# Optimization experiments

Hardware: AMD Instinct MI355X
Metric: run time of the kernel (lower is better)

Reference implementation:

```python
import jax, jax.numpy as jnp
from jax import lax
import numpy as np

B, N, NPOINT, NSAMPLE, C = 4, 8192, 2048, 32, 128
RADIUS = 0.2
H1, H2, OUT = 64, 128, 128  # mlp: (3+C)->H1->H2, sas: H2->OUT


def fps(xyz, npoint):
    # furthest point sampling: xyz (B,N,3) -> idx (B,npoint) int32
    b, n, _ = xyz.shape
    init_idx = jnp.zeros((b,), jnp.int32)

    def step(carry, _):
        dist, last = carry
        p = jnp.take_along_axis(xyz, last[:, None, None], axis=1)  # (B,1,3)
        d = jnp.sum((xyz - p) ** 2, axis=-1)                       # (B,N)
        dist = jnp.minimum(dist, d)
        nxt = jnp.argmax(dist, axis=-1).astype(jnp.int32)
        return (dist, nxt), nxt

    (_, _), rest = lax.scan(step, (jnp.full((b, n), 1e10, jnp.float32), init_idx),
                            None, length=npoint - 1)
    return jnp.concatenate([init_idx[None, :], rest], axis=0).T    # (B,npoint)


def ball_query(xyz, new_xyz, radius, nsample):
    # xyz (B,N,3), new_xyz (B,S,3) -> idx (B,S,nsample) int32
    n = xyz.shape[1]
    d2 = jnp.sum((new_xyz[:, :, None, :] - xyz[:, None, :, :]) ** 2, axis=-1)  # (B,S,N)
    ar = jnp.arange(n, dtype=jnp.int32)
    keys = jnp.where(d2 <= radius * radius, ar, n)  # valid -> own index, invalid -> N
    neg_vals, _ = lax.top_k(-keys, nsample)          # smallest nsample keys
    idx = -neg_vals
    first = idx[..., :1]
    return jnp.where(idx >= n, first, idx)           # pad invalid with first valid


def gather_points(pts, idx):
    # pts (B,N,D), idx (B,S,ns) -> (B,S,ns,D)
    b, s, ns = idx.shape
    flat = jnp.take_along_axis(pts, idx.reshape(b, s * ns, 1), axis=1)
    return flat.reshape(b, s, ns, -1)


def setup_inputs() -> dict:
    key = jax.random.key(0)
    ks = jax.random.split(key, 8)
    xyz = jax.random.uniform(ks[0], (B, N, 3), dtype=jnp.float32)
    features = jax.random.normal(ks[1], (B, C, N), dtype=jnp.float32)
    cin = C + 3
    W1 = jax.random.normal(ks[2], (H1, cin), dtype=jnp.float32) / np.sqrt(cin)
    b1 = jnp.zeros((H1,), jnp.float32)
    W2 = jax.random.normal(ks[3], (H2, H1), dtype=jnp.float32) / np.sqrt(H1)
    b2 = jnp.zeros((H2,), jnp.float32)
    Wsa = jax.random.normal(ks[4], (OUT, H2), dtype=jnp.float32) / np.sqrt(H2)
    bsa = jnp.zeros((OUT,), jnp.float32)
    return {"xyz": xyz, "features": features, "W1": W1, "b1": b1,
            "W2": W2, "b2": b2, "Wsa": Wsa, "bsa": bsa}


def reference(xyz, features, W1, b1, W2, b2, Wsa, bsa):
    center_idx = fps(xyz, NPOINT)                                   # (B,S)
    new_xyz = jnp.take_along_axis(xyz, center_idx[:, :, None], axis=1)  # (B,S,3)
    g_idx = ball_query(xyz, new_xyz, RADIUS, NSAMPLE)               # (B,S,ns)
    g_xyz = gather_points(xyz, g_idx) - new_xyz[:, :, None, :]      # (B,S,ns,3) relative coords
    g_feat = gather_points(features.transpose(0, 2, 1), g_idx)      # (B,S,ns,C)
    h = jnp.concatenate([g_xyz, g_feat], axis=-1)                   # (B,S,ns,3+C)
    h = jax.nn.relu(jnp.einsum('bsnc,oc->bsno', h, W1) + b1)        # shared 1x1-conv MLP
    h = jax.nn.relu(jnp.einsum('bsnc,oc->bsno', h, W2) + b2)
    pooled = jnp.max(h, axis=2)                                     # max over nsample -> (B,S,H2)
    out = jnp.einsum('bsc,oc->bso', pooled, Wsa) + bsa              # sas channel mixer
    return new_xyz, out.transpose(0, 2, 1)                          # (B,S,3), (B,OUT,S)
```

## Files before the change

kernel.cpp:

```cpp
#include <hip/hip_runtime.h>
#include <cstdint>
#include <cstddef>

#define NB 4
#define NN 8192
#define NPTS 2048
#define NSAMP 32
#define NC 128
#define CIN 131
#define NH1 64
#define NH2 128
#define NOUTC 128
#define GCELLS 4096

typedef float v2f __attribute__((ext_vector_type(2)));

__device__ __forceinline__ float d2_exact(float ax, float ay, float az,
                                          float bx, float by, float bz) {
  float dx = ax - bx, dy = ay - by, dz = az - bz;
  return __fadd_rn(__fadd_rn(__fmul_rn(dx, dx), __fmul_rn(dy, dy)),
                   __fmul_rn(dz, dz));
}

#if __has_builtin(__builtin_amdgcn_mov_dpp)
template <int CTRL>
__device__ __forceinline__ float dppf(float v) {
  return __int_as_float(
      __builtin_amdgcn_mov_dpp(__float_as_int(v), CTRL, 0xF, 0xF, true));
}
template <int CTRL>
__device__ __forceinline__ int dppi(int v) {
  return __builtin_amdgcn_mov_dpp(v, CTRL, 0xF, 0xF, true);
}
#else
template <int CTRL>
__device__ __forceinline__ float dppf(float v) {
  const int m = (CTRL == 0xB1) ? 1 : (CTRL == 0x4E) ? 2 : (CTRL == 0x141) ? 7 : 15;
  return __shfl_xor(v, m);
}
template <int CTRL>
__device__ __forceinline__ int dppi(int v) {
  const int m = (CTRL == 0xB1) ? 1 : (CTRL == 0x4E) ? 2 : (CTRL == 0x141) ? 7 : 15;
  return __shfl_xor(v, m);
}
#endif

__device__ __forceinline__ void red_pair(float& bv, int& bi, float ov, int oi) {
  bool t = (ov > bv) || (ov == bv && oi < bi);
  bv = t ? ov : bv;
  bi = t ? oi : bi;
}
__device__ __forceinline__ void red3(float& bv, int& bi, int& bs,
                                     float ov, int oi, int os) {
  bool t = (ov > bv) || (ov == bv && oi < bi);
  bv = t ? ov : bv;
  bi = t ? oi : bi;
  bs = t ? os : bs;
}

__device__ __forceinline__ int spread3(int v) {
  return (v & 1) | ((v & 2) << 2) | ((v & 4) << 4) | ((v & 8) << 6);
}

__global__ __launch_bounds__(1024, 1) void sort_kernel(
    const float* __restrict__ xyz, float* __restrict__ xs,
    float* __restrict__ ys, float* __restrict__ zs, int* __restrict__ io) {
  __shared__ int hist[GCELLS];
  __shared__ int cbase[GCELLS];
  __shared__ int wtot[16];
  __shared__ int woff[16];
  const int b = blockIdx.x;
  const int tid = threadIdx.x;
  const int lane = tid & 63;
  const int wid = tid >> 6;
  const float* xb = xyz + (size_t)b * NN * 3;
  for (int i = tid; i < GCELLS; i += 1024) hist[i] = 0;
  __syncthreads();
  int cell[8];
  float px[8], py[8], pz[8];
#pragma unroll
  for (int k = 0; k < 8; ++k) {
    int j = tid + (k << 10);
    float x = xb[j * 3 + 0], y = xb[j * 3 + 1], z = xb[j * 3 + 2];
    px[k] = x; py[k] = y; pz[k] = z;
    int cx = min(15, max(0, (int)(x * 16.0f)));
    int cy = min(15, max(0, (int)(y * 16.0f)));
    int cz = min(15, max(0, (int)(z * 16.0f)));
    cell[k] = spread3(cx) | (spread3(cy) << 1) | (spread3(cz) << 2);
    atomicAdd(&hist[cell[k]], 1);
  }
  __syncthreads();
  const int i0 = tid * 4;
  int h0 = hist[i0], h1 = hist[i0 + 1], h2 = hist[i0 + 2], h3 = hist[i0 + 3];
  int s4 = h0 + h1 + h2 + h3;
  int v = s4;
#pragma unroll
  for (int d = 1; d < 64; d <<= 1) {
    int o = __shfl_up(v, d);
    if (lane >= d) v += o;
  }
  if (lane == 63) wtot[wid] = v;
  __syncthreads();
  if (tid < 16) {
    int acc = 0;
    for (int w = 0; w < 16; ++w) {
      if (w == tid) woff[tid] = acc;
      acc += wtot[w];
    }
  }
  __syncthreads();
  int eb = woff[wid] + v - s4;
  cbase[i0] = eb;
  cbase[i0 + 1] = eb + h0;
  cbase[i0 + 2] = eb + h0 + h1;
  cbase[i0 + 3] = eb + h0 + h1 + h2;
  __syncthreads();
  for (int i = tid; i < GCELLS; i += 1024) hist[i] = 0;
  __syncthreads();
  const size_t bo = (size_t)b * NN;
#pragma unroll
  for (int k = 0; k < 8; ++k) {
    int pos = cbase[cell[k]] + atomicAdd(&hist[cell[k]], 1);
    xs[bo + pos] = px[k];
    ys[bo + pos] = py[k];
    zs[bo + pos] = pz[k];
    io[bo + pos] = tid + (k << 10);
  }
}

__global__ __launch_bounds__(512, 1) void fps_kernel(
    const float* __restrict__ xyz, const float* __restrict__ xs,
    const float* __restrict__ ys, const float* __restrict__ zs,
    const int* __restrict__ io, float* __restrict__ newxyz) {
#pragma clang fp contract(off)
  const int b = blockIdx.x;
  const int tid = threadIdx.x;
  const int lane = tid & 63;
  const int wid = tid >> 6;
  const size_t bo = (size_t)b * NN;

  float X[2][8], Y[2][8], Z[2][8], D[2][8];
  int I[2][8];
  float GCX[2], GCY[2], GCZ[2], GR[2];
  float GV[2], GX[2], GY[2], GZ[2];
  int GI[2];
#pragma unroll
  for (int p = 0; p < 2; ++p) {
    float mx = 0.f, my = 0.f, mz = 0.f;
#pragma unroll
    for (int k = 0; k < 8; ++k) {
      int s = p * 4096 + tid * 8 + k;
      X[p][k] = xs[bo + s];
      Y[p][k] = ys[bo + s];
      Z[p][k] = zs[bo + s];
      I[p][k] = io[bo + s];
      D[p][k] = 1e10f;
      mx += X[p][k]; my += Y[p][k]; mz += Z[p][k];
    }
    mx *= 0.125f; my *= 0.125f; mz *= 0.125f;
    float r2m = 0.f;
#pragma unroll
    for (int k = 0; k < 8; ++k)
      r2m = fmaxf(r2m, d2_exact(X[p][k], Y[p][k], Z[p][k], mx, my, mz));
    GCX[p] = mx; GCY[p] = my; GCZ[p] = mz;
    GR[p] = __fmul_rn(sqrtf(r2m), 1.0001f) + 1e-6f;
    GV[p] = 1e10f;
    GI[p] = I[p][0]; GX[p] = X[p][0]; GY[p] = Y[p][0]; GZ[p] = Z[p][0];
  }

  __shared__ float vbuf[2][8];
  __shared__ int ibuf[2][8];
  __shared__ float cbuf[2][8][3];

  const float* xb = xyz + (size_t)b * NN * 3;
  float cx = xb[0], cy = xb[1], cz = xb[2];
  if (tid == 0) {
    newxyz[(size_t)b * NPTS * 3 + 0] = cx;
    newxyz[(size_t)b * NPTS * 3 + 1] = cy;
    newxyz[(size_t)b * NPTS * 3 + 2] = cz;
  }

  for (int t = 1; t < NPTS; ++t) {
    const int par = t & 1;
#pragma unroll
    for (int p = 0; p < 2; ++p) {
      float d2c = d2_exact(GCX[p], GCY[p], GCZ[p], cx, cy, cz);
      float lb = sqrtf(d2c) - GR[p];
      float lbm = lb - 1e-3f;
      bool skip = (lb > 2e-3f) && (__fmul_rn(lbm, lbm) >= GV[p]);
      if (!skip) {
        float gv = -1.f; int gi = 0;
        float gx = 0.f, gy = 0.f, gz = 0.f;
#pragma unroll
        for (int k = 0; k < 8; ++k) {
          float d2 = d2_exact(X[p][k], Y[p][k], Z[p][k], cx, cy, cz);
          float nd = fminf(D[p][k], d2);
          D[p][k] = nd;
          bool c = (nd > gv) || (nd == gv && I[p][k] < gi);
          gv = c ? nd : gv; gi = c ? I[p][k] : gi;
          gx = c ? X[p][k] : gx; gy = c ? Y[p][k] : gy; gz = c ? Z[p][k] : gz;
        }
        GV[p] = gv; GI[p] = gi; GX[p] = gx; GY[p] = gy; GZ[p] = gz;
      }
    }
    float bv = GV[0]; int bi = GI[0];
    float bx = GX[0], by = GY[0], bz = GZ[0];
    {
      bool c = (GV[1] > bv) || (GV[1] == bv && GI[1] < bi);
      bv = c ? GV[1] : bv; bi = c ? GI[1] : bi;
      bx = c ? GX[1] : bx; by = c ? GY[1] : by; bz = c ? GZ[1] : bz;
    }
    float rv = bv; int ri = bi;
    red_pair(rv, ri, dppf<0xB1>(rv), dppi<0xB1>(ri));
    red_pair(rv, ri, dppf<0x4E>(rv), dppi<0x4E>(ri));
    red_pair(rv, ri, dppf<0x141>(rv), dppi<0x141>(ri));
    red_pair(rv, ri, dppf<0x140>(rv), dppi<0x140>(ri));
    red_pair(rv, ri, __shfl_xor(rv, 16), __shfl_xor(ri, 16));
    red_pair(rv, ri, __shfl_xor(rv, 32), __shfl_xor(ri, 32));
    if (bi == ri) {
      vbuf[par][wid] = rv;
      ibuf[par][wid] = ri;
      cbuf[par][wid][0] = bx; cbuf[par][wid][1] = by; cbuf[par][wid][2] = bz;
    }
    __syncthreads();
    int sl = lane & 7;
    float v2 = vbuf[par][sl];
    int i2 = ibuf[par][sl];
    int s2 = sl;
    red3(v2, i2, s2, dppf<0xB1>(v2), dppi<0xB1>(i2), dppi<0xB1>(s2));
    red3(v2, i2, s2, dppf<0x4E>(v2), dppi<0x4E>(i2), dppi<0x4E>(s2));
    red3(v2, i2, s2, dppf<0x141>(v2), dppi<0x141>(i2), dppi<0x141>(s2));
    cx = cbuf[par][s2][0]; cy = cbuf[par][s2][1]; cz = cbuf[par][s2][2];
    if (bi == i2) {
      size_t o = ((size_t)b * NPTS + t) * 3;
      newxyz[o + 0] = bx; newxyz[o + 1] = by; newxyz[o + 2] = bz;
    }
  }
}

__global__ __launch_bounds__(1024, 1) void fps_nosort_kernel(
    const float* __restrict__ xyz, float* __restrict__ newxyz) {
#pragma clang fp contract(off)
  const int b = blockIdx.x;
  const int tid = threadIdx.x;
  const int lane = tid & 63;
  const int wid = tid >> 6;
  const float* xb = xyz + (size_t)b * NN * 3;
  v2f x2[4], y2[4], z2[4], dd[4];
#pragma unroll
  for (int p = 0; p < 4; ++p) {
    int j0 = tid + ((2 * p) << 10);
    int j1 = tid + ((2 * p + 1) << 10);
    x2[p].x = xb[j0 * 3 + 0]; x2[p].y = xb[j1 * 3 + 0];
    y2[p].x = xb[j0 * 3 + 1]; y2[p].y = xb[j1 * 3 + 1];
    z2[p].x = xb[j0 * 3 + 2]; z2[p].y = xb[j1 * 3 + 2];
    dd[p].x = 1e10f; dd[p].y = 1e10f;
  }
  __shared__ float vbuf[2][16];
  __shared__ int ibuf[2][16];
  __shared__ float cbuf[2][16][3];
  float cx = xb[0], cy = xb[1], cz = xb[2];
  if (tid == 0) {
    newxyz[(size_t)b * NPTS * 3 + 0] = cx;
    newxyz[(size_t)b * NPTS * 3 + 1] = cy;
    newxyz[(size_t)b * NPTS * 3 + 2] = cz;
  }
  for (int t = 1; t < NPTS; ++t) {
    const int par = t & 1;
    float bv = -1.0f; int bi = 0;
    float bwx = 0.f, bwy = 0.f, bwz = 0.f;
#pragma unroll
    for (int p = 0; p < 4; ++p) {
      v2f dx = x2[p] - (v2f){cx, cx};
      v2f dy = y2[p] - (v2f){cy, cy};
      v2f dz = z2[p] - (v2f){cz, cz};
      v2f s = dx * dx + dy * dy + dz * dz;
      v2f nd;
      nd.x = fminf(dd[p].x, s.x);
      nd.y = fminf(dd[p].y, s.y);
      dd[p] = nd;
      { bool c = nd.x > bv;
        bv = c ? nd.x : bv; bi = c ? (tid + ((2 * p) << 10)) : bi;
        bwx = c ? x2[p].x : bwx; bwy = c ? y2[p].x : bwy; bwz = c ? z2[p].x : bwz; }
      { bool c = nd.y > bv;
        bv = c ? nd.y : bv; bi = c ? (tid + ((2 * p + 1) << 10)) : bi;
        bwx = c ? x2[p].y : bwx; bwy = c ? y2[p].y : bwy; bwz = c ? z2[p].y : bwz; }
    }
    red_pair(bv, bi, dppf<0xB1>(bv), dppi<0xB1>(bi));
    red_pair(bv, bi, dppf<0x4E>(bv), dppi<0x4E>(bi));
    red_pair(bv, bi, dppf<0x141>(bv), dppi<0x141>(bi));
    red_pair(bv, bi, dppf<0x140>(bv), dppi<0x140>(bi));
    red_pair(bv, bi, __shfl_xor(bv, 16), __shfl_xor(bi, 16));
    red_pair(bv, bi, __shfl_xor(bv, 32), __shfl_xor(bi, 32));
    if (tid == (bi & 1023)) {
      vbuf[par][wid] = bv; ibuf[par][wid] = bi;
      cbuf[par][wid][0] = bwx; cbuf[par][wid][1] = bwy; cbuf[par][wid][2] = bwz;
    }
    __syncthreads();
    float v2w = vbuf[par][lane & 15];
    int i2w = ibuf[par][lane & 15];
    red_pair(v2w, i2w, dppf<0xB1>(v2w), dppi<0xB1>(i2w));
    red_pair(v2w, i2w, dppf<0x4E>(v2w), dppi<0x4E>(i2w));
    red_pair(v2w, i2w, dppf<0x141>(v2w), dppi<0x141>(i2w));
    red_pair(v2w, i2w, dppf<0x140>(v2w), dppi<0x140>(i2w));
    const int slot = (i2w & 1023) >> 6;
    cx = cbuf[par][slot][0]; cy = cbuf[par][slot][1]; cz = cbuf[par][slot][2];
    if (tid == (i2w & 1023)) {
      size_t o = ((size_t)b * NPTS + t) * 3;
      newxyz[o + 0] = cx; newxyz[o + 1] = cy; newxyz[o + 2] = cz;
    }
  }
}

__global__ __launch_bounds__(256) void ballq_kernel(
    const float* __restrict__ xyz, const float* __restrict__ newxyz,
    int* __restrict__ bidx) {
  const int cid = blockIdx.x * 4 + (threadIdx.x >> 6);
  const int lane = threadIdx.x & 63;
  const int b = cid >> 11;
  const float* xb = xyz + (size_t)b * NN * 3;
  const float cx = newxyz[(size_t)cid * 3 + 0];
  const float cy = newxyz[(size_t)cid * 3 + 1];
  const float cz = newxyz[(size_t)cid * 3 + 2];
  int* ob = bidx + (size_t)cid * NSAMP;
  int total = 0;
  int first = -1;
  for (int c0 = 0; c0 < NN; c0 += 64) {
    int j = c0 + lane;
    float xx = xb[j * 3 + 0], yy = xb[j * 3 + 1], zz = xb[j * 3 + 2];
    float d2 = d2_exact(cx, cy, cz, xx, yy, zz);
    bool in = d2 <= 0.04f;
    unsigned long long m = __ballot(in);
    if (first < 0 && m) first = c0 + __builtin_ctzll(m);
    int pos = total + __popcll(m & ((1ull << lane) - 1ull));
    if (in && pos < NSAMP) ob[pos] = j;
    total += __popcll(m);
    if (total >= NSAMP) break;
  }
  if (total < NSAMP && lane < NSAMP - total) ob[total + lane] = first;
}

__global__ void tw_kernel(const float* __restrict__ W1, const float* __restrict__ W2,
                          const float* __restrict__ Wsa, float* __restrict__ w1t,
                          float* __restrict__ w2t, float* __restrict__ wsat) {
  int i = blockIdx.x * blockDim.x + threadIdx.x;
  if (i < CIN * NH1) w1t[i] = W1[(i % NH1) * CIN + (i / NH1)];
  if (i < NH1 * NH2) w2t[i] = W2[(i % NH2) * NH1 + (i / NH2)];
  if (i < NH2 * NOUTC) wsat[i] = Wsa[(i % NOUTC) * NH2 + (i / NOUTC)];
}

__global__ void tfeat_kernel(const float* __restrict__ feat, float* __restrict__ featT) {
  __shared__ float tile[32][33];
  const int b = blockIdx.z;
  const int n0 = blockIdx.x * 32, c0 = blockIdx.y * 32;
  const int tx = threadIdx.x, ty = threadIdx.y;
#pragma unroll
  for (int r = 0; r < 4; ++r)
    tile[ty + r * 8][tx] = feat[((size_t)b * NC + c0 + ty + r * 8) * NN + n0 + tx];
  __syncthreads();
#pragma unroll
  for (int r = 0; r < 4; ++r)
    featT[((size_t)b * NN + n0 + ty + r * 8) * NC + c0 + tx] = tile[tx][ty + r * 8];
}

#define HS 36
__global__ __launch_bounds__(256) void mlp_kernel(
    const float* __restrict__ xyz, const float* __restrict__ fsrc,
    const float* __restrict__ newxyz, const int* __restrict__ bidx,
    const float* __restrict__ w1t, const float* __restrict__ b1,
    const float* __restrict__ w2t, const float* __restrict__ b2,
    const float* __restrict__ wsat, const float* __restrict__ bsa,
    float* __restrict__ out1, int useT) {
  __shared__ float h[CIN * HS];
  __shared__ float h1[NH1 * HS];
  __shared__ float pl[256];
  __shared__ float pooled[NH2];
  __shared__ int sidx[NSAMP];
  __shared__ float sc[3];
  const int cid = blockIdx.x;
  const int b = cid >> 11;
  const int s = cid & 2047;
  const int tid = threadIdx.x;
  if (tid < NSAMP) sidx[tid] = bidx[(size_t)cid * NSAMP + tid];
  if (tid < 3) sc[tid] = newxyz[(size_t)cid * 3 + tid];
  __syncthreads();
  {
    const int ss = tid >> 3, q = tid & 7;
    const int j = sidx[ss];
    if (useT) {
      const float4* fr = (const float4*)(fsrc + ((size_t)b * NN + j) * NC + q * 16);
#pragma unroll
      for (int u = 0; u < 4; ++u) {
        float4 v = fr[u];
        int c = 3 + q * 16 + u * 4;
        h[(c + 0) * HS + ss] = v.x;
        h[(c + 1) * HS + ss] = v.y;
        h[(c + 2) * HS + ss] = v.z;
        h[(c + 3) * HS + ss] = v.w;
      }
    } else {
      for (int u = 0; u < 16; ++u) {
        int c = q * 16 + u;
        h[(3 + c) * HS + ss] = fsrc[((size_t)b * NC + c) * NN + j];
      }
    }
    if (q == 0) {
      const float* pr = xyz + ((size_t)b * NN + j) * 3;
      h[0 * HS + ss] = pr[0] - sc[0];
      h[1 * HS + ss] = pr[1] - sc[1];
      h[2 * HS + ss] = pr[2] - sc[2];
    }
  }
  __syncthreads();
  {
    const int o = tid & 63, sg = tid >> 6;
    float acc[8];
    const float bb = b1[o];
#pragma unroll
    for (int i = 0; i < 8; ++i) acc[i] = bb;
    const float4* hb = (const float4*)&h[sg * 8];
    for (int k = 0; k < CIN; ++k) {
      float w = w1t[k * NH1 + o];
      float4 a = hb[k * (HS / 4) + 0];
      float4 c = hb[k * (HS / 4) + 1];
      acc[0] = fmaf(w, a.x, acc[0]); acc[1] = fmaf(w, a.y, acc[1]);
      acc[2] = fmaf(w, a.z, acc[2]); acc[3] = fmaf(w, a.w, acc[3]);
      acc[4] = fmaf(w, c.x, acc[4]); acc[5] = fmaf(w, c.y, acc[5]);
      acc[6] = fmaf(w, c.z, acc[6]); acc[7] = fmaf(w, c.w, acc[7]);
    }
#pragma unroll
    for (int i = 0; i < 8; ++i) h1[o * HS + sg * 8 + i] = fmaxf(acc[i], 0.0f);
  }
  __syncthreads();
  {
    const int o = tid & 127, sg = tid >> 7;
    float acc[16];
    const float bb = b2[o];
#pragma unroll
    for (int i = 0; i < 16; ++i) acc[i] = bb;
    const float4* hb = (const float4*)&h1[sg * 16];
    for (int k = 0; k < NH1; ++k) {
      float w = w2t[k * NH2 + o];
#pragma unroll
      for (int u = 0; u < 4; ++u) {
        float4 a = hb[k * (HS / 4) + u];
        acc[u * 4 + 0] = fmaf(w, a.x, acc[u * 4 + 0]);
        acc[u * 4 + 1] = fmaf(w, a.y, acc[u * 4 + 1]);
        acc[u * 4 + 2] = fmaf(w, a.z, acc[u * 4 + 2]);
        acc[u * 4 + 3] = fmaf(w, a.w, acc[u * 4 + 3]);
      }
    }
    float pm = acc[0];
#pragma unroll
    for (int i = 1; i < 16; ++i) pm = fmaxf(pm, acc[i]);
    pl[sg * 128 + o] = pm;
  }
  __syncthreads();
  if (tid < NH2) pooled[tid] = fmaxf(fmaxf(pl[tid], pl[128 + tid]), 0.0f);
  __syncthreads();
  if (tid < NOUTC) {
    float acc = bsa[tid];
    for (int k = 0; k < NH2; ++k) acc = fmaf(pooled[k], wsat[k * NOUTC + tid], acc);
    out1[((size_t)b * NOUTC + tid) * NPTS + s] = acc;
  }
}

extern "C" void kernel_launch(void* const* d_in, const int* in_sizes, int n_in,
                              void* d_out, int out_size, void* d_ws, size_t ws_size,
                              hipStream_t stream) {
  const float* xyz = (const float*)d_in[0];
  const float* feat = (const float*)d_in[1];
  const float* W1 = (const float*)d_in[2];
  const float* b1 = (const float*)d_in[3];
  const float* W2 = (const float*)d_in[4];
  const float* b2 = (const float*)d_in[5];
  const float* Wsa = (const float*)d_in[6];
  const float* bsa = (const float*)d_in[7];
  float* out = (float*)d_out;
  float* newxyz = out;
  float* out1 = out + (size_t)NB * NPTS * 3;

  const size_t sort_f = (size_t)NB * NN * 4;
  const size_t small_f = (size_t)CIN * NH1 + NH1 * NH2 + NH2 * NOUTC +
                         (size_t)NB * NPTS * NSAMP;
  const size_t featT_f = (size_t)NB * NN * NC;

  float* ws = (float*)d_ws;
  bool useSort = ws_size >= (sort_f + small_f) * 4;
  bool useT = ws_size >= (sort_f + small_f + featT_f) * 4;

  float* xs = ws;
  float* ysr = xs + (size_t)NB * NN;
  float* zsr = ysr + (size_t)NB * NN;
  int* iosr = (int*)(zsr + (size_t)NB * NN);
  float* base2 = useSort ? (ws + sort_f) : ws;
  float* w1t = base2;
  float* w2t = w1t + CIN * NH1;
  float* wsat = w2t + NH1 * NH2;
  int* bidx = (int*)(wsat + NH2 * NOUTC);
  float* featT = (float*)(bidx + (size_t)NB * NPTS * NSAMP);

  tw_kernel<<<64, 256, 0, stream>>>(W1, W2, Wsa, w1t, w2t, wsat);
  if (useT)
    tfeat_kernel<<<dim3(NN / 32, NC / 32, NB), dim3(32, 8), 0, stream>>>(feat, featT);
  if (useSort) {
    sort_kernel<<<NB, 1024, 0, stream>>>(xyz, xs, ysr, zsr, iosr);
    fps_kernel<<<NB, 512, 0, stream>>>(xyz, xs, ysr, zsr, iosr, newxyz);
  } else {
    fps_nosort_kernel<<<NB, 1024, 0, stream>>>(xyz, newxyz);
  }
  ballq_kernel<<<NB * NPTS / 4, 256, 0, stream>>>(xyz, newxyz, bidx);
  mlp_kernel<<<NB * NPTS, 256, 0, stream>>>(xyz, useT ? featT : feat, newxyz, bidx,
                                            w1t, b1, w2t, b2, wsat, bsa, out1,
                                            (int)useT);
}
```

Measured before the change: 4.168 ms.

## Restructure FPS to 1024 threads with cached per-thread maxima and skip-aware wave reduction

The FPS kernel now runs 1024 threads, each holding one group of 8 sorted points instead of two. Each thread keeps a threshold T derived from its current max distance and its group radius, and recomputes distances only when the new centre falls within that bound. Whole waves skip the intra-wave argmax reduction when no lane is dirty and reuse their cached result. The winner's coordinates are fetched with a lane shuffle, and the cross-wave reduction now carries coordinates through DPP over 16 waves. This targets the serial per-iteration latency, at the cost of a wider block barrier and extra DPP traffic in the final reduction.

```diff
diff --git a/kernel.cpp b/kernel.cpp
--- a/kernel.cpp
+++ b/kernel.cpp
@@ -50,12 +50,15 @@
   bv = t ? ov : bv;
   bi = t ? oi : bi;
 }
-__device__ __forceinline__ void red3(float& bv, int& bi, int& bs,
-                                     float ov, int oi, int os) {
-  bool t = (ov > bv) || (ov == bv && oi < bi);
-  bv = t ? ov : bv;
-  bi = t ? oi : bi;
-  bs = t ? os : bs;
+template <int CTRL>
+__device__ __forceinline__ void red5(float& v, int& i, float& x, float& y,
+                                     float& z) {
+  float ov = dppf<CTRL>(v);
+  int oi = dppi<CTRL>(i);
+  float ox = dppf<CTRL>(x), oy = dppf<CTRL>(y), oz = dppf<CTRL>(z);
+  bool t = (ov > v) || (ov == v && oi < i);
+  v = t ? ov : v; i = t ? oi : i;
+  x = t ? ox : x; y = t ? oy : y; z = t ? oz : z;
 }
 
 __device__ __forceinline__ int spread3(int v) {
@@ -123,12 +126,12 @@
     int pos = cbase[cell[k]] + atomicAdd(&hist[cell[k]], 1);
     xs[bo + pos] = px[k];
     ys[bo + pos] = py[k];
-    zs[bo + pos] = pz[k];
+    zs[bo + pos] = zs == nullptr ? 0.f : pz[k];
     io[bo + pos] = tid + (k << 10);
   }
 }
 
-__global__ __launch_bounds__(512, 1) void fps_kernel(
+__global__ __launch_bounds__(1024, 1) void fps_kernel(
     const float* __restrict__ xyz, const float* __restrict__ xs,
     const float* __restrict__ ys, const float* __restrict__ zs,
     const int* __restrict__ io, float* __restrict__ newxyz) {
@@ -139,38 +142,39 @@
   const int wid = tid >> 6;
   const size_t bo = (size_t)b * NN;
 
-  float X[2][8], Y[2][8], Z[2][8], D[2][8];
-  int I[2][8];
-  float GCX[2], GCY[2], GCZ[2], GR[2];
-  float GV[2], GX[2], GY[2], GZ[2];
-  int GI[2];
-#pragma unroll
-  for (int p = 0; p < 2; ++p) {
+  float X[8], Y[8], Z[8], D[8];
+  int I[8];
+  float gcx, gcy, gcz, gr;
+  {
     float mx = 0.f, my = 0.f, mz = 0.f;
 #pragma unroll
     for (int k = 0; k < 8; ++k) {
-      int s = p * 4096 + tid * 8 + k;
-      X[p][k] = xs[bo + s];
-      Y[p][k] = ys[bo + s];
-      Z[p][k] = zs[bo + s];
-      I[p][k] = io[bo + s];
-      D[p][k] = 1e10f;
-      mx += X[p][k]; my += Y[p][k]; mz += Z[p][k];
+      int s = tid * 8 + k;
+      X[k] = xs[bo + s];
+      Y[k] = ys[bo + s];
+      Z[k] = zs[bo + s];
+      I[k] = io[bo + s];
+      D[k] = 1e30f;
+      mx += X[k]; my += Y[k]; mz += Z[k];
     }
     mx *= 0.125f; my *= 0.125f; mz *= 0.125f;
     float r2m = 0.f;
 #pragma unroll
     for (int k = 0; k < 8; ++k)
-      r2m = fmaxf(r2m, d2_exact(X[p][k], Y[p][k], Z[p][k], mx, my, mz));
-    GCX[p] = mx; GCY[p] = my; GCZ[p] = mz;
-    GR[p] = __fmul_rn(sqrtf(r2m), 1.0001f) + 1e-6f;
-    GV[p] = 1e10f;
-    GI[p] = I[p][0]; GX[p] = X[p][0]; GY[p] = Y[p][0]; GZ[p] = Z[p][0];
-  }
-
-  __shared__ float vbuf[2][8];
-  __shared__ int ibuf[2][8];
-  __shared__ float cbuf[2][8][3];
+      r2m = fmaxf(r2m, d2_exact(X[k], Y[k], Z[k], mx, my, mz));
+    gcx = mx; gcy = my; gcz = mz;
+    gr = __fmul_rn(sqrtf(r2m), 1.0001f) + 1e-6f;
+  }
+  float gv = -1.0f;
+  int gidx = 0x3fffffff;
+  float bwx = 0.f, bwy = 0.f, bwz = 0.f;
+  float T = 3e38f;
+  float cv = -1.0f; int ci = 0x3fffffff;
+  float ccx = 0.f, ccy = 0.f, ccz = 0.f;
+
+  __shared__ float sv[2][16];
+  __shared__ int si[2][16];
+  __shared__ float sxx[2][16], syy[2][16], szz[2][16];
 
   const float* xb = xyz + (size_t)b * NN * 3;
   float cx = xb[0], cy = xb[1], cz = xb[2];
@@ -182,58 +186,56 @@
 
   for (int t = 1; t < NPTS; ++t) {
     const int par = t & 1;
-#pragma unroll
-    for (int p = 0; p < 2; ++p) {
-      float d2c = d2_exact(GCX[p], GCY[p], GCZ[p], cx, cy, cz);
-      float lb = sqrtf(d2c) - GR[p];
-      float lbm = lb - 1e-3f;
-      bool skip = (lb > 2e-3f) && (__fmul_rn(lbm, lbm) >= GV[p]);
-      if (!skip) {
-        float gv = -1.f; int gi = 0;
-        float gx = 0.f, gy = 0.f, gz = 0.f;
-#pragma unroll
-        for (int k = 0; k < 8; ++k) {
-          float d2 = d2_exact(X[p][k], Y[p][k], Z[p][k], cx, cy, cz);
-          float nd = fminf(D[p][k], d2);
-          D[p][k] = nd;
-          bool c = (nd > gv) || (nd == gv && I[p][k] < gi);
-          gv = c ? nd : gv; gi = c ? I[p][k] : gi;
-          gx = c ? X[p][k] : gx; gy = c ? Y[p][k] : gy; gz = c ? Z[p][k] : gz;
-        }
-        GV[p] = gv; GI[p] = gi; GX[p] = gx; GY[p] = gy; GZ[p] = gz;
+    const float d2c = d2_exact(gcx, gcy, gcz, cx, cy, cz);
+    const bool dirty = d2c < T;
+    if (dirty) {
+      float nv = -1.0f; int ni = 0x3fffffff;
+      float nx = 0.f, ny = 0.f, nz = 0.f;
+#pragma unroll
+      for (int k = 0; k < 8; ++k) {
+        float d2 = d2_exact(X[k], Y[k], Z[k], cx, cy, cz);
+        float nd = fminf(D[k], d2);
+        D[k] = nd;
+        bool c = (nd > nv) || (nd == nv && I[k] < ni);
+        nv = c ? nd : nv; ni = c ? I[k] : ni;
+        nx = c ? X[k] : nx; ny = c ? Y[k] : ny; nz = c ? Z[k] : nz;
       }
-    }
-    float bv = GV[0]; int bi = GI[0];
-    float bx = GX[0], by = GY[0], bz = GZ[0];
-    {
-      bool c = (GV[1] > bv) || (GV[1] == bv && GI[1] < bi);
-      bv = c ? GV[1] : bv; bi = c ? GI[1] : bi;
-      bx = c ? GX[1] : bx; by = c ? GY[1] : by; bz = c ? GZ[1] : bz;
-    }
-    float rv = bv; int ri = bi;
-    red_pair(rv, ri, dppf<0xB1>(rv), dppi<0xB1>(ri));
-    red_pair(rv, ri, dppf<0x4E>(rv), dppi<0x4E>(ri));
-    red_pair(rv, ri, dppf<0x141>(rv), dppi<0x141>(ri));
-    red_pair(rv, ri, dppf<0x140>(rv), dppi<0x140>(ri));
-    red_pair(rv, ri, __shfl_xor(rv, 16), __shfl_xor(ri, 16));
-    red_pair(rv, ri, __shfl_xor(rv, 32), __shfl_xor(ri, 32));
-    if (bi == ri) {
-      vbuf[par][wid] = rv;
-      ibuf[par][wid] = ri;
-      cbuf[par][wid][0] = bx; cbuf[par][wid][1] = by; cbuf[par][wid][2] = bz;
+      gv = nv; gidx = ni; bwx = nx; bwy = ny; bwz = nz;
+      float s = __fadd_rn(__fmul_rn(sqrtf(nv), 1.0001f), __fadd_rn(gr, 2e-3f));
+      T = __fmul_rn(__fmul_rn(s, s), 1.0001f);
+    }
+    if (__ballot(dirty) != 0ull) {
+      float rv = gv; int ri = gidx;
+      red_pair(rv, ri, dppf<0xB1>(rv), dppi<0xB1>(ri));
+      red_pair(rv, ri, dppf<0x4E>(rv), dppi<0x4E>(ri));
+      red_pair(rv, ri, dppf<0x141>(rv), dppi<0x141>(ri));
+      red_pair(rv, ri, dppf<0x140>(rv), dppi<0x140>(ri));
+      red_pair(rv, ri, __shfl_xor(rv, 16), __shfl_xor(ri, 16));
+      red_pair(rv, ri, __shfl_xor(rv, 32), __shfl_xor(ri, 32));
+      unsigned long long m = __ballot(gidx == ri);
+      int owner = (int)__builtin_ctzll(m);
+      cv = rv; ci = ri;
+      ccx = __shfl(bwx, owner);
+      ccy = __shfl(bwy, owner);
+      ccz = __shfl(bwz, owner);
+    }
+    if (lane == 0) {
+      sv[par][wid] = cv; si[par][wid] = ci;
+      sxx[par][wid] = ccx; syy[par][wid] = ccy; szz[par][wid] = ccz;
     }
     __syncthreads();
-    int sl = lane & 7;
-    float v2 = vbuf[par][sl];
-    int i2 = ibuf[par][sl];
-    int s2 = sl;
-    red3(v2, i2, s2, dppf<0xB1>(v2), dppi<0xB1>(i2), dppi<0xB1>(s2));
-    red3(v2, i2, s2, dppf<0x4E>(v2), dppi<0x4E>(i2), dppi<0x4E>(s2));
-    red3(v2, i2, s2, dppf<0x141>(v2), dppi<0x141>(i2), dppi<0x141>(s2));
-    cx = cbuf[par][s2][0]; cy = cbuf[par][s2][1]; cz = cbuf[par][s2][2];
-    if (bi == i2) {
+    const int sl = lane & 15;
+    float v = sv[par][sl];
+    int i = si[par][sl];
+    float xx = sxx[par][sl], yy = syy[par][sl], zz = szz[par][sl];
+    red5<0xB1>(v, i, xx, yy, zz);
+    red5<0x4E>(v, i, xx, yy, zz);
+    red5<0x141>(v, i, xx, yy, zz);
+    red5<0x140>(v, i, xx, yy, zz);
+    cx = xx; cy = yy; cz = zz;
+    if (gidx == i) {
       size_t o = ((size_t)b * NPTS + t) * 3;
-      newxyz[o + 0] = bx; newxyz[o + 1] = by; newxyz[o + 2] = bz;
+      newxyz[o + 0] = xx; newxyz[o + 1] = yy; newxyz[o + 2] = zz;
     }
   }
 }
@@ -505,7 +507,7 @@
     tfeat_kernel<<<dim3(NN / 32, NC / 32, NB), dim3(32, 8), 0, stream>>>(feat, featT);
   if (useSort) {
     sort_kernel<<<NB, 1024, 0, stream>>>(xyz, xs, ysr, zsr, iosr);
-    fps_kernel<<<NB, 512, 0, stream>>>(xyz, xs, ysr, zsr, iosr, newxyz);
+    fps_kernel<<<NB, 1024, 0, stream>>>(xyz, xs, ysr, zsr, iosr, newxyz);
   } else {
     fps_nosort_kernel<<<NB, 1024, 0, stream>>>(xyz, newxyz);
   }
```

New measurement: 4.096 ms. Within noise of the previous version (-1.7%).
